# Kernel optimization log

Hardware: AMD Instinct MI355X
Metric: run time of the kernel (lower is better)

Reference implementation:

```python
import jax, jax.numpy as jnp
import numpy as np

NUM_DIM = 384
NUM_HEADS = 12
WIN = 7
L = WIN * WIN
NW = 4
B_ = 1024

def _relative_coords():
    ch, cw = np.meshgrid(np.arange(WIN), np.arange(WIN), indexing='ij')
    coords = np.stack([ch, cw]).reshape(2, -1)  # (2, L)
    rel = coords[:, :, None] - coords[:, None, :]  # (2, L, L)
    rel[0] += WIN - 1
    rel[1] += WIN - 1
    rel[0] *= 2 * WIN - 1
    return jnp.asarray(rel.sum(0), dtype=jnp.int32)  # (L, L)

def setup_inputs() -> dict:
    key = jax.random.key(0)
    k_x, k_m, k_qkv, k_pw, k_pb, k_rb = jax.random.split(key, 6)
    x = jax.random.normal(k_x, (B_, L, NUM_DIM), dtype=jnp.float32)
    mask = jax.random.bernoulli(k_m, 0.5, (NW, L, L))
    qkv_w = jax.random.normal(k_qkv, (3 * NUM_DIM, NUM_DIM), dtype=jnp.float32) * (NUM_DIM ** -0.5)
    proj_w = jax.random.normal(k_pw, (NUM_DIM, NUM_DIM), dtype=jnp.float32) * (NUM_DIM ** -0.5)
    proj_b = jax.random.normal(k_pb, (NUM_DIM,), dtype=jnp.float32) * 0.02
    rel_bias = jax.random.normal(k_rb, ((2 * WIN - 1) * (2 * WIN - 1), NUM_HEADS), dtype=jnp.float32) * 0.2
    rel_coords = _relative_coords()
    return {"x": x, "mask": mask, "qkv_w": qkv_w, "proj_w": proj_w,
            "proj_b": proj_b, "rel_bias": rel_bias, "rel_coords": rel_coords}

def reference(x, mask, qkv_w, proj_w, proj_b, rel_bias, rel_coords):
    Bt, Lx, C = x.shape
    H = NUM_HEADS
    hd = C // H
    scale = float(C) ** 0.5  # faithful: original multiplies by num_dim**0.5
    qkv = (x @ qkv_w.T).reshape(Bt, Lx, 3, H, hd).transpose(2, 0, 3, 1, 4)
    q, k, v = qkv[0], qkv[1], qkv[2]  # each (B_, H, L, hd)
    attn = jnp.einsum('bhqd,bhkd->bhqk', q, k) * scale
    bias = rel_bias[rel_coords].transpose(2, 0, 1)  # (H, L, L)
    attn = attn + bias[None]
    nw = mask.shape[0]
    attn = attn.reshape(-1, nw, H, Lx, Lx)
    attn = jnp.where(mask[None, :, None], jnp.float32(-100.0), attn)
    attn = attn.reshape(Bt, H, Lx, Lx)
    attn = jax.nn.softmax(attn, axis=-1)
    out = jnp.einsum('bhqk,bhkd->bhqd', attn, v)  # (B_, H, L, hd)
    out = out.transpose(0, 2, 1, 3).reshape(Bt, Lx, C)
    return out @ proj_w.T + proj_b
```

## Files before the change

### kernel.cpp

```cpp
#include <hip/hip_runtime.h>
#include <math.h>

#define NUM_B 1024
#define LW 49
#define CD 384
#define NH 12
#define HD 32
#define SCALE_F 19.595917942265423f

typedef unsigned short u16;
typedef unsigned int u32;
typedef __attribute__((ext_vector_type(8))) short short8;
typedef __attribute__((ext_vector_type(8))) _Float16 half8;
typedef __attribute__((ext_vector_type(4))) float floatx4;

static __device__ __forceinline__ u16 f2bf(float f) {
    unsigned u = __float_as_uint(f);
    u += 0x7fffu + ((u >> 16) & 1u);
    return (u16)(u >> 16);
}
static __device__ __forceinline__ float bf2f(u16 s) {
    return __uint_as_float(((unsigned)s) << 16);
}
static __device__ __forceinline__ u16 f2h_bits(float f) {
    _Float16 h = (_Float16)f;
    u16 u;
    __builtin_memcpy(&u, &h, 2);
    return u;
}
static __device__ __forceinline__ void gl_lds16(const u16* g, u16* l) {
    __builtin_amdgcn_global_load_lds(
        (const __attribute__((address_space(1))) void*)g,
        (__attribute__((address_space(3))) void*)l, 16, 0, 0);
}

#define X4 4816896
#define W4 110592
#define P4 36864
#define BM4 49152
__global__ __launch_bounds__(256) void prep(const float* __restrict__ x,
                                            const float* __restrict__ qkv_w,
                                            const float* __restrict__ proj_w,
                                            const float* __restrict__ rel_bias,
                                            const int* __restrict__ rel_coords,
                                            const int* __restrict__ mask,
                                            u16* __restrict__ xbh, u16* __restrict__ xbl,
                                            u16* __restrict__ wbh, u16* __restrict__ wbl,
                                            u16* __restrict__ pfh, u16* __restrict__ pfl,
                                            float* __restrict__ bm) {
    int idx = blockIdx.x * 256 + threadIdx.x;
    if (idx < X4) {
        float4 v = ((const float4*)x)[idx];
        ushort4 h, l;
        h.x = f2bf(v.x); l.x = f2bf(v.x - bf2f(h.x));
        h.y = f2bf(v.y); l.y = f2bf(v.y - bf2f(h.y));
        h.z = f2bf(v.z); l.z = f2bf(v.z - bf2f(h.z));
        h.w = f2bf(v.w); l.w = f2bf(v.w - bf2f(h.w));
        ((ushort4*)xbh)[idx] = h;
        ((ushort4*)xbl)[idx] = l;
    } else if (idx < X4 + W4) {
        int i = idx - X4;
        float4 v = ((const float4*)qkv_w)[i];
        ushort4 h, l;
        h.x = f2bf(v.x); l.x = f2bf(v.x - bf2f(h.x));
        h.y = f2bf(v.y); l.y = f2bf(v.y - bf2f(h.y));
        h.z = f2bf(v.z); l.z = f2bf(v.z - bf2f(h.z));
        h.w = f2bf(v.w); l.w = f2bf(v.w - bf2f(h.w));
        ((ushort4*)wbh)[i] = h;
        ((ushort4*)wbl)[i] = l;
    } else if (idx < X4 + W4 + P4) {
        int i = idx - (X4 + W4);
        float4 v = ((const float4*)proj_w)[i];
        ushort4 h, l;
        h.x = f2h_bits(v.x); l.x = f2h_bits(v.x - (float)(_Float16)v.x);
        h.y = f2h_bits(v.y); l.y = f2h_bits(v.y - (float)(_Float16)v.y);
        h.z = f2h_bits(v.z); l.z = f2h_bits(v.z - (float)(_Float16)v.z);
        h.w = f2h_bits(v.w); l.w = f2h_bits(v.w - (float)(_Float16)v.w);
        ((ushort4*)pfh)[i] = h;
        ((ushort4*)pfl)[i] = l;
    } else if (idx < X4 + W4 + P4 + BM4) {
        int t = idx - (X4 + W4 + P4);
        float4 o;
        float* op = (float*)&o;
#pragma unroll
        for (int i = 0; i < 4; ++i) {
            int j = t * 4 + i;
            int e = j & 63;
            int col = (e & 3) * 16 + (e >> 2);
            int row = (j >> 6) & 63;
            int wh_ = j >> 12;
            int w = wh_ / NH;
            int h = wh_ - w * NH;
            float val = -1.0e30f;
            if (row < LW && col < LW) {
                int ij = row * LW + col;
                val = mask[w * (LW * LW) + ij] ? -1.0e4f
                                               : rel_bias[rel_coords[ij] * NH + h];
            }
            op[i] = val;
        }
        ((float4*)bm)[t] = o;
    }
}

__global__ __launch_bounds__(256) void qkv_gemm(const u16* __restrict__ Ah,
                                                const u16* __restrict__ Al,
                                                const u16* __restrict__ Wh,
                                                const u16* __restrict__ Wl,
                                                u32* __restrict__ qp,
                                                u32* __restrict__ kp,
                                                u16* __restrict__ vp) {
    __shared__ u16 As_h[2][128 * 32];
    __shared__ u16 As_l[2][128 * 32];
    __shared__ u16 Bs_h[2][128 * 32];
    __shared__ u16 Bs_l[2][128 * 32];
    const int tid = threadIdx.x;
    const int w = tid >> 6;
    const int lane = tid & 63;
    const int bid = blockIdx.x;
    const int logical = (bid & 7) * 441 + (bid >> 3);
    const int mt = logical / 9;
    const int nt = logical - mt * 9;
    const int m0 = mt * 128;
    const int n0 = nt * 128;
    const bool vblk = (nt >= 6);
    const int quad = lane >> 4;
    const int lc = lane & 15;
    const int wrow = (w >> 1) << 6;
    const int wcol = (w & 1) << 6;
    const int srow = lane >> 2;
    const int sch = (lane & 3) * 8;

    floatx4 acc[4][4];
#pragma unroll
    for (int a = 0; a < 4; ++a)
#pragma unroll
        for (int b = 0; b < 4; ++b) acc[a][b] = (floatx4){0.f, 0.f, 0.f, 0.f};

    auto stage = [&](int buf, int k0) {
#pragma unroll
        for (int i = 0; i < 2; ++i) {
            const int rb = w * 32 + i * 16;
            const size_t ga = (size_t)(m0 + rb + srow) * CD + k0 + sch;
            const size_t gb = (size_t)(n0 + rb + srow) * CD + k0 + sch;
            const int lof = rb * 32;
            gl_lds16(Ah + ga, As_h[buf] + lof);
            gl_lds16(Wh + gb, Bs_h[buf] + lof);
            if (!vblk) {
                gl_lds16(Al + ga, As_l[buf] + lof);
                gl_lds16(Wl + gb, Bs_l[buf] + lof);
            }
        }
    };

    auto compute = [&](int buf) {
        if (!vblk) {
            short8 af_h[4], af_l[4], bf_h[4], bf_l[4];
#pragma unroll
            for (int t = 0; t < 4; ++t) {
                const int ar = (wrow + t * 16 + lc) * 32 + quad * 8;
                af_h[t] = *(const short8*)(As_h[buf] + ar);
                af_l[t] = *(const short8*)(As_l[buf] + ar);
                const int br = (wcol + t * 16 + lc) * 32 + quad * 8;
                bf_h[t] = *(const short8*)(Bs_h[buf] + br);
                bf_l[t] = *(const short8*)(Bs_l[buf] + br);
            }
#pragma unroll
            for (int tm = 0; tm < 4; ++tm)
#pragma unroll
                for (int tn = 0; tn < 4; ++tn) {
                    acc[tm][tn] = __builtin_amdgcn_mfma_f32_16x16x32_bf16(af_h[tm], bf_h[tn], acc[tm][tn], 0, 0, 0);
                    acc[tm][tn] = __builtin_amdgcn_mfma_f32_16x16x32_bf16(af_h[tm], bf_l[tn], acc[tm][tn], 0, 0, 0);
                    acc[tm][tn] = __builtin_amdgcn_mfma_f32_16x16x32_bf16(af_l[tm], bf_h[tn], acc[tm][tn], 0, 0, 0);
                }
        } else {
            short8 af_h[4], bf_h[4];
#pragma unroll
            for (int t = 0; t < 4; ++t) {
                af_h[t] = *(const short8*)(As_h[buf] + (wrow + t * 16 + lc) * 32 + quad * 8);
                bf_h[t] = *(const short8*)(Bs_h[buf] + (wcol + t * 16 + lc) * 32 + quad * 8);
            }
#pragma unroll
            for (int tm = 0; tm < 4; ++tm)
#pragma unroll
                for (int tn = 0; tn < 4; ++tn)
                    acc[tm][tn] = __builtin_amdgcn_mfma_f32_16x16x32_bf16(af_h[tm], bf_h[tn], acc[tm][tn], 0, 0, 0);
        }
    };

    stage(0, 0);
    __syncthreads();
    for (int t = 0; t < 12; t += 2) {
        stage(1, (t + 1) * 32);
        compute(0);
        __syncthreads();
        if (t + 2 < 12) stage(0, (t + 2) * 32);
        compute(1);
        __syncthreads();
    }

#pragma unroll
    for (int tn = 0; tn < 4; ++tn) {
        const int nst = n0 + wcol + tn * 16;
        const int t = nst / CD;
        const int rem = nst - t * CD;
        const int h = rem >> 5;
        const int db = (rem & 31) + lc;
#pragma unroll
        for (int tm = 0; tm < 4; ++tm)
#pragma unroll
            for (int r = 0; r < 4; ++r) {
                const int m = m0 + wrow + tm * 16 + quad * 4 + r;
                const int b = m / LW;
                const int l = m - b * LW;
                const size_t o = ((((size_t)b * NH + h) * LW + l) << 5) + db;
                const float vv = acc[tm][tn][r];
                if (t == 2) {
                    vp[o] = f2h_bits(vv);
                } else {
                    const unsigned bits = __float_as_uint(vv);
                    const unsigned hi_high = bits & 0xffff0000u;
                    const u16 lo = f2bf(vv - __uint_as_float(hi_high));
                    const u32 packed = hi_high | (u32)lo;
                    if (t == 0) qp[o] = packed; else kp[o] = packed;
                }
            }
    }
}

__global__ __launch_bounds__(256) void proj_gemm(const u16* __restrict__ Af,
                                                 const u16* __restrict__ Wfh,
                                                 const u16* __restrict__ Wfl,
                                                 const float* __restrict__ pb,
                                                 float* __restrict__ outF) {
    __shared__ u16 As_f[2][128 * 32];
    __shared__ u16 Bs_h[2][128 * 32];
    __shared__ u16 Bs_l[2][128 * 32];
    const int tid = threadIdx.x;
    const int w = tid >> 6;
    const int lane = tid & 63;
    const int bid = blockIdx.x;
    const int logical = (bid & 7) * 147 + (bid >> 3);
    const int mt = logical / 3;
    const int nt = logical - mt * 3;
    const int m0 = mt * 128;
    const int n0 = nt * 128;
    const int quad = lane >> 4;
    const int lc = lane & 15;
    const int wrow = (w >> 1) << 6;
    const int wcol = (w & 1) << 6;
    const int srow = lane >> 2;
    const int sch = (lane & 3) * 8;

    floatx4 acc[4][4];
#pragma unroll
    for (int a = 0; a < 4; ++a)
#pragma unroll
        for (int b = 0; b < 4; ++b) acc[a][b] = (floatx4){0.f, 0.f, 0.f, 0.f};

    auto stage = [&](int buf, int k0) {
#pragma unroll
        for (int i = 0; i < 2; ++i) {
            const int rb = w * 32 + i * 16;
            const size_t ga = (size_t)(m0 + rb + srow) * CD + k0 + sch;
            const size_t gb = (size_t)(n0 + rb + srow) * CD + k0 + sch;
            const int lof = rb * 32;
            gl_lds16(Af + ga, As_f[buf] + lof);
            gl_lds16(Wfh + gb, Bs_h[buf] + lof);
            gl_lds16(Wfl + gb, Bs_l[buf] + lof);
        }
    };

    auto compute = [&](int buf) {
        half8 af[4], bh[4], bl[4];
#pragma unroll
        for (int t = 0; t < 4; ++t) {
            af[t] = *(const half8*)(As_f[buf] + (wrow + t * 16 + lc) * 32 + quad * 8);
            const int br = (wcol + t * 16 + lc) * 32 + quad * 8;
            bh[t] = *(const half8*)(Bs_h[buf] + br);
            bl[t] = *(const half8*)(Bs_l[buf] + br);
        }
#pragma unroll
        for (int tm = 0; tm < 4; ++tm)
#pragma unroll
            for (int tn = 0; tn < 4; ++tn) {
                acc[tm][tn] = __builtin_amdgcn_mfma_f32_16x16x32_f16(af[tm], bh[tn], acc[tm][tn], 0, 0, 0);
                acc[tm][tn] = __builtin_amdgcn_mfma_f32_16x16x32_f16(af[tm], bl[tn], acc[tm][tn], 0, 0, 0);
            }
    };

    stage(0, 0);
    __syncthreads();
    for (int t = 0; t < 12; t += 2) {
        stage(1, (t + 1) * 32);
        compute(0);
        __syncthreads();
        if (t + 2 < 12) stage(0, (t + 2) * 32);
        compute(1);
        __syncthreads();
    }

#pragma unroll
    for (int tn = 0; tn < 4; ++tn) {
        const int n = n0 + wcol + tn * 16 + lc;
        const float bias = pb[n];
#pragma unroll
        for (int tm = 0; tm < 4; ++tm)
#pragma unroll
            for (int r = 0; r < 4; ++r) {
                const int m = m0 + wrow + tm * 16 + quad * 4 + r;
                outF[(size_t)m * CD + n] = acc[tm][tn][r] + bias;
            }
    }
}

__global__ __launch_bounds__(64) void attn_mfma(const u32* __restrict__ qp,
                                                const u32* __restrict__ kp,
                                                const u16* __restrict__ vh,
                                                const float* __restrict__ bm,
                                                u16* __restrict__ aof) {
    const int bh = blockIdx.x;
    const int b = bh / NH;
    const int h = bh - b * NH;
    const int lane = threadIdx.x;
    const int quad = lane >> 4;
    const int lc = lane & 15;
    __shared__ u16 Vt[32 * 72];
    __shared__ u16 Ps[64 * 72];

    const size_t base = (size_t)bh * (LW * HD);

    short8 aQh[4], aQl[4], bKh[4], bKl[4];
#pragma unroll
    for (int t = 0; t < 4; ++t) {
        int row = t * 16 + lc; if (row > 48) row = 48;
        const size_t o = base + (size_t)row * HD + quad * 8;
        uint4 q0 = *(const uint4*)(qp + o);
        uint4 q1 = *(const uint4*)(qp + o + 4);
        uint4 k0 = *(const uint4*)(kp + o);
        uint4 k1 = *(const uint4*)(kp + o + 4);
        unsigned qv[8] = {q0.x, q0.y, q0.z, q0.w, q1.x, q1.y, q1.z, q1.w};
        unsigned kv[8] = {k0.x, k0.y, k0.z, k0.w, k1.x, k1.y, k1.z, k1.w};
#pragma unroll
        for (int e = 0; e < 8; ++e) {
            aQh[t][e] = (short)(qv[e] >> 16);
            aQl[t][e] = (short)(qv[e] & 0xffffu);
            bKh[t][e] = (short)(kv[e] >> 16);
            bKl[t][e] = (short)(kv[e] & 0xffffu);
        }
    }
#pragma unroll
    for (int it = 0; it < 4; ++it) {
        const int idx = lane + it * 64;
        const int j = idx >> 2;
        const int jc = j > 48 ? 48 : j;
        const int ch = (idx & 3) * 8;
        short8 vv = *(const short8*)(vh + base + (size_t)jc * HD + ch);
#pragma unroll
        for (int e = 0; e < 8; ++e) Vt[(ch + e) * 72 + j] = (u16)vv[e];
    }

    floatx4 acc[4][4];
#pragma unroll
    for (int a = 0; a < 4; ++a)
#pragma unroll
        for (int c = 0; c < 4; ++c) acc[a][c] = (floatx4){0.f, 0.f, 0.f, 0.f};
#pragma unroll
    for (int tm = 0; tm < 4; ++tm)
#pragma unroll
        for (int tn = 0; tn < 4; ++tn) {
            acc[tm][tn] = __builtin_amdgcn_mfma_f32_16x16x32_bf16(aQh[tm], bKh[tn], acc[tm][tn], 0, 0, 0);
            acc[tm][tn] = __builtin_amdgcn_mfma_f32_16x16x32_bf16(aQh[tm], bKl[tn], acc[tm][tn], 0, 0, 0);
            acc[tm][tn] = __builtin_amdgcn_mfma_f32_16x16x32_bf16(aQl[tm], bKh[tn], acc[tm][tn], 0, 0, 0);
        }

    const float* bmp = bm + (((size_t)(b & 3) * NH + h) << 12);
#pragma unroll
    for (int tm = 0; tm < 4; ++tm)
#pragma unroll
        for (int r = 0; r < 4; ++r) {
            const int row = tm * 16 + quad * 4 + r;
            const float4 bv = *(const float4*)(bmp + row * 64 + lc * 4);
            const float s0 = fmaf(acc[tm][0][r], SCALE_F, bv.x);
            const float s1 = fmaf(acc[tm][1][r], SCALE_F, bv.y);
            const float s2 = fmaf(acc[tm][2][r], SCALE_F, bv.z);
            const float s3 = fmaf(acc[tm][3][r], SCALE_F, bv.w);
            float mx = fmaxf(fmaxf(s0, s1), fmaxf(s2, s3));
#pragma unroll
            for (int off = 1; off < 16; off <<= 1) mx = fmaxf(mx, __shfl_xor(mx, off));
            const float e0 = __expf(s0 - mx);
            const float e1 = __expf(s1 - mx);
            const float e2 = __expf(s2 - mx);
            const float e3 = __expf(s3 - mx);
            float sum = (e0 + e1) + (e2 + e3);
#pragma unroll
            for (int off = 1; off < 16; off <<= 1) sum += __shfl_xor(sum, off);
            const float inv = __builtin_amdgcn_rcpf(sum);
            Ps[row * 72 +  0 + lc] = f2h_bits(e0 * inv);
            Ps[row * 72 + 16 + lc] = f2h_bits(e1 * inv);
            Ps[row * 72 + 32 + lc] = f2h_bits(e2 * inv);
            Ps[row * 72 + 48 + lc] = f2h_bits(e3 * inv);
        }

    __syncthreads();

    floatx4 o[4][2];
#pragma unroll
    for (int a = 0; a < 4; ++a) { o[a][0] = (floatx4){0.f,0.f,0.f,0.f}; o[a][1] = (floatx4){0.f,0.f,0.f,0.f}; }
#pragma unroll
    for (int ks = 0; ks < 2; ++ks) {
        const half8 bV0 = *(const half8*)(Vt + (lc) * 72 + ks * 32 + quad * 8);
        const half8 bV1 = *(const half8*)(Vt + (16 + lc) * 72 + ks * 32 + quad * 8);
#pragma unroll
        for (int tm = 0; tm < 4; ++tm) {
            const half8 aP = *(const half8*)(Ps + (tm * 16 + lc) * 72 + ks * 32 + quad * 8);
            o[tm][0] = __builtin_amdgcn_mfma_f32_16x16x32_f16(aP, bV0, o[tm][0], 0, 0, 0);
            o[tm][1] = __builtin_amdgcn_mfma_f32_16x16x32_f16(aP, bV1, o[tm][1], 0, 0, 0);
        }
    }
#pragma unroll
    for (int tm = 0; tm < 4; ++tm)
#pragma unroll
        for (int r = 0; r < 4; ++r) {
            const int i = tm * 16 + quad * 4 + r;
            if (i < LW) {
#pragma unroll
                for (int tn = 0; tn < 2; ++tn) {
                    const size_t mm = ((size_t)b * LW + i) * CD + h * HD + tn * 16 + lc;
                    aof[mm] = f2h_bits(o[tm][tn][r]);
                }
            }
        }
}

extern "C" void kernel_launch(void* const* d_in, const int* in_sizes, int n_in,
                              void* d_out, int out_size, void* d_ws, size_t ws_size,
                              hipStream_t stream) {
    const float* x          = (const float*)d_in[0];
    const int*   mask       = (const int*)d_in[1];
    const float* qkv_w      = (const float*)d_in[2];
    const float* proj_w     = (const float*)d_in[3];
    const float* proj_b     = (const float*)d_in[4];
    const float* rel_bias   = (const float*)d_in[5];
    const int*   rel_coords = (const int*)d_in[6];
    float* out = (float*)d_out;

    const size_t S = (size_t)NUM_B * NH * LW * HD;
    u16* xbh = (u16*)d_ws;
    u16* xbl = xbh + S;
    u32* kp  = (u32*)(xbl + S);
    u16* vh  = (u16*)(kp + S);
    u16* wbh = vh + S;
    u16* wbl = wbh + 442368;
    u16* pfh = wbl + 442368;
    u16* pfl = pfh + 147456;
    float* bm = (float*)(pfl + 147456);
    u32* qp = (u32*)d_out;
    u16* aof = xbh;

    prep<<<dim3(19584), dim3(256), 0, stream>>>(x, qkv_w, proj_w, rel_bias, rel_coords,
                                                mask, xbh, xbl, wbh, wbl, pfh, pfl, bm);
    qkv_gemm<<<dim3(3528), dim3(256), 0, stream>>>(xbh, xbl, wbh, wbl, qp, kp, vh);
    attn_mfma<<<dim3(NUM_B * NH), dim3(64), 0, stream>>>(qp, kp, vh, bm, aof);
    proj_gemm<<<dim3(1176), dim3(256), 0, stream>>>(aof, pfh, pfl, proj_b, out);
}
```

Measured before the change: 404.5 us.

## Deepen GEMM double-buffer pipeline with explicit vmcnt waits and raw barriers

Both GEMM kernels now issue loads for the first two k-tiles up front and prefetch the next tile into a buffer right after it has been consumed. __syncthreads is replaced with hand-placed s_waitcnt vmcnt/lgkmcnt and s_barrier, so only the older stage's global-to-LDS loads must land before compute. The aim is to keep two tiles of loads in flight and overlap them with the MFMA work. The vmcnt constants are hard-coded to the number of loads each stage issues (different for the vblk path), so a mismatch would silently read incomplete LDS data.

```diff
diff --git a/kernel.cpp b/kernel.cpp
--- a/kernel.cpp
+++ b/kernel.cpp
@@ -13,6 +13,10 @@
 typedef __attribute__((ext_vector_type(8))) short short8;
 typedef __attribute__((ext_vector_type(8))) _Float16 half8;
 typedef __attribute__((ext_vector_type(4))) float floatx4;
+
+#define ASM_VMCNT(n) asm volatile("s_waitcnt vmcnt(" #n ")" ::: "memory")
+#define ASM_LGKM0()  asm volatile("s_waitcnt lgkmcnt(0)" ::: "memory")
+#define BAR()        __builtin_amdgcn_s_barrier()
 
 static __device__ __forceinline__ u16 f2bf(float f) {
     unsigned u = __float_as_uint(f);
@@ -189,14 +193,33 @@
     };
 
     stage(0, 0);
-    __syncthreads();
-    for (int t = 0; t < 12; t += 2) {
-        stage(1, (t + 1) * 32);
-        compute(0);
-        __syncthreads();
-        if (t + 2 < 12) stage(0, (t + 2) * 32);
-        compute(1);
-        __syncthreads();
+    stage(1, 32);
+    if (!vblk) {
+#pragma unroll
+        for (int t = 0; t < 12; t += 2) {
+            ASM_VMCNT(8); BAR();
+            compute(0);
+            ASM_LGKM0(); BAR();
+            if (t + 2 < 12) { stage(0, (t + 2) * 32); ASM_VMCNT(8); }
+            else            { ASM_VMCNT(0); }
+            BAR();
+            compute(1);
+            ASM_LGKM0(); BAR();
+            if (t + 2 < 12) stage(1, (t + 3) * 32);
+        }
+    } else {
+#pragma unroll
+        for (int t = 0; t < 12; t += 2) {
+            ASM_VMCNT(4); BAR();
+            compute(0);
+            ASM_LGKM0(); BAR();
+            if (t + 2 < 12) { stage(0, (t + 2) * 32); ASM_VMCNT(4); }
+            else            { ASM_VMCNT(0); }
+            BAR();
+            compute(1);
+            ASM_LGKM0(); BAR();
+            if (t + 2 < 12) stage(1, (t + 3) * 32);
+        }
     }
 
 #pragma unroll
@@ -290,14 +313,18 @@
     };
 
     stage(0, 0);
-    __syncthreads();
+    stage(1, 32);
+#pragma unroll
     for (int t = 0; t < 12; t += 2) {
-        stage(1, (t + 1) * 32);
+        ASM_VMCNT(6); BAR();
         compute(0);
-        __syncthreads();
-        if (t + 2 < 12) stage(0, (t + 2) * 32);
+        ASM_LGKM0(); BAR();
+        if (t + 2 < 12) { stage(0, (t + 2) * 32); ASM_VMCNT(6); }
+        else            { ASM_VMCNT(0); }
+        BAR();
         compute(1);
-        __syncthreads();
+        ASM_LGKM0(); BAR();
+        if (t + 2 < 12) stage(1, (t + 3) * 32);
     }
 
 #pragma unroll
```

After: 388.0 us. 4.1% less time.

## Triple-buffer GEMM LDS staging and load low-part operands directly from global

Applied to the files above, without the earlier changes.

Both the QKV and projection GEMMs move from double buffering with two __syncthreads per pair of steps to a three-stage ring. Each k-step now uses an explicit vmcnt wait and one barrier, and keeps two stages of loads in flight. The low-precision correction operands (Al/Wl, Wfl) no longer go through LDS and are read straight from global memory into registers. Launch bounds request three blocks per CU. This cuts LDS footprint and barrier stalls, at the cost of uncoalesced per-lane global reads for the low parts and hand-counted vmcnt that must match the number of outstanding loads.

```diff
diff --git a/kernel.cpp b/kernel.cpp
--- a/kernel.cpp
+++ b/kernel.cpp
@@ -13,6 +13,9 @@
 typedef __attribute__((ext_vector_type(8))) short short8;
 typedef __attribute__((ext_vector_type(8))) _Float16 half8;
 typedef __attribute__((ext_vector_type(4))) float floatx4;
+
+#define ASM_VMCNT(n) asm volatile("s_waitcnt vmcnt(" #n ")" ::: "memory")
+#define BAR()        __builtin_amdgcn_s_barrier()
 
 static __device__ __forceinline__ u16 f2bf(float f) {
     unsigned u = __float_as_uint(f);
@@ -103,17 +106,15 @@
     }
 }
 
-__global__ __launch_bounds__(256) void qkv_gemm(const u16* __restrict__ Ah,
-                                                const u16* __restrict__ Al,
-                                                const u16* __restrict__ Wh,
-                                                const u16* __restrict__ Wl,
-                                                u32* __restrict__ qp,
-                                                u32* __restrict__ kp,
-                                                u16* __restrict__ vp) {
-    __shared__ u16 As_h[2][128 * 32];
-    __shared__ u16 As_l[2][128 * 32];
-    __shared__ u16 Bs_h[2][128 * 32];
-    __shared__ u16 Bs_l[2][128 * 32];
+__global__ __launch_bounds__(256, 3) void qkv_gemm(const u16* __restrict__ Ah,
+                                                   const u16* __restrict__ Al,
+                                                   const u16* __restrict__ Wh,
+                                                   const u16* __restrict__ Wl,
+                                                   u32* __restrict__ qp,
+                                                   u32* __restrict__ kp,
+                                                   u16* __restrict__ vp) {
+    __shared__ u16 As_h[3][128 * 32];
+    __shared__ u16 Bs_h[3][128 * 32];
     const int tid = threadIdx.x;
     const int w = tid >> 6;
     const int lane = tid & 63;
@@ -141,44 +142,53 @@
 #pragma unroll
         for (int i = 0; i < 2; ++i) {
             const int rb = w * 32 + i * 16;
-            const size_t ga = (size_t)(m0 + rb + srow) * CD + k0 + sch;
-            const size_t gb = (size_t)(n0 + rb + srow) * CD + k0 + sch;
-            const int lof = rb * 32;
-            gl_lds16(Ah + ga, As_h[buf] + lof);
-            gl_lds16(Wh + gb, Bs_h[buf] + lof);
-            if (!vblk) {
-                gl_lds16(Al + ga, As_l[buf] + lof);
-                gl_lds16(Wl + gb, Bs_l[buf] + lof);
-            }
+            gl_lds16(Ah + (size_t)(m0 + rb + srow) * CD + k0 + sch, As_h[buf] + rb * 32);
+            gl_lds16(Wh + (size_t)(n0 + rb + srow) * CD + k0 + sch, Bs_h[buf] + rb * 32);
         }
     };
 
-    auto compute = [&](int buf) {
+    stage(0, 0);
+    stage(1, 32);
+
+#pragma unroll
+    for (int t = 0; t < 12; ++t) {
+        if (t == 11) { ASM_VMCNT(0); } else { ASM_VMCNT(4); }
+        BAR();
+        const int buf = t % 3;
+        const int k0 = t * 32;
         if (!vblk) {
-            short8 af_h[4], af_l[4], bf_h[4], bf_l[4];
-#pragma unroll
-            for (int t = 0; t < 4; ++t) {
-                const int ar = (wrow + t * 16 + lc) * 32 + quad * 8;
-                af_h[t] = *(const short8*)(As_h[buf] + ar);
-                af_l[t] = *(const short8*)(As_l[buf] + ar);
-                const int br = (wcol + t * 16 + lc) * 32 + quad * 8;
-                bf_h[t] = *(const short8*)(Bs_h[buf] + br);
-                bf_l[t] = *(const short8*)(Bs_l[buf] + br);
+            short8 af_l[4], bf_l[4];
+#pragma unroll
+            for (int tt = 0; tt < 4; ++tt) {
+                af_l[tt] = *(const short8*)(Al + (size_t)(m0 + wrow + tt * 16 + lc) * CD + k0 + quad * 8);
+                bf_l[tt] = *(const short8*)(Wl + (size_t)(n0 + wcol + tt * 16 + lc) * CD + k0 + quad * 8);
+            }
+            if (t + 2 < 12) stage((t + 2) % 3, (t + 2) * 32);
+            short8 af_h[4], bf_h[4];
+#pragma unroll
+            for (int tt = 0; tt < 4; ++tt) {
+                af_h[tt] = *(const short8*)(As_h[buf] + (wrow + tt * 16 + lc) * 32 + quad * 8);
+                bf_h[tt] = *(const short8*)(Bs_h[buf] + (wcol + tt * 16 + lc) * 32 + quad * 8);
             }
 #pragma unroll
             for (int tm = 0; tm < 4; ++tm)
 #pragma unroll
+                for (int tn = 0; tn < 4; ++tn)
+                    acc[tm][tn] = __builtin_amdgcn_mfma_f32_16x16x32_bf16(af_h[tm], bf_h[tn], acc[tm][tn], 0, 0, 0);
+#pragma unroll
+            for (int tm = 0; tm < 4; ++tm)
+#pragma unroll
                 for (int tn = 0; tn < 4; ++tn) {
-                    acc[tm][tn] = __builtin_amdgcn_mfma_f32_16x16x32_bf16(af_h[tm], bf_h[tn], acc[tm][tn], 0, 0, 0);
                     acc[tm][tn] = __builtin_amdgcn_mfma_f32_16x16x32_bf16(af_h[tm], bf_l[tn], acc[tm][tn], 0, 0, 0);
                     acc[tm][tn] = __builtin_amdgcn_mfma_f32_16x16x32_bf16(af_l[tm], bf_h[tn], acc[tm][tn], 0, 0, 0);
                 }
         } else {
+            if (t + 2 < 12) stage((t + 2) % 3, (t + 2) * 32);
             short8 af_h[4], bf_h[4];
 #pragma unroll
-            for (int t = 0; t < 4; ++t) {
-                af_h[t] = *(const short8*)(As_h[buf] + (wrow + t * 16 + lc) * 32 + quad * 8);
-                bf_h[t] = *(const short8*)(Bs_h[buf] + (wcol + t * 16 + lc) * 32 + quad * 8);
+            for (int tt = 0; tt < 4; ++tt) {
+                af_h[tt] = *(const short8*)(As_h[buf] + (wrow + tt * 16 + lc) * 32 + quad * 8);
+                bf_h[tt] = *(const short8*)(Bs_h[buf] + (wcol + tt * 16 + lc) * 32 + quad * 8);
             }
 #pragma unroll
             for (int tm = 0; tm < 4; ++tm)
@@ -186,17 +196,6 @@
                 for (int tn = 0; tn < 4; ++tn)
                     acc[tm][tn] = __builtin_amdgcn_mfma_f32_16x16x32_bf16(af_h[tm], bf_h[tn], acc[tm][tn], 0, 0, 0);
         }
-    };
-
-    stage(0, 0);
-    __syncthreads();
-    for (int t = 0; t < 12; t += 2) {
-        stage(1, (t + 1) * 32);
-        compute(0);
-        __syncthreads();
-        if (t + 2 < 12) stage(0, (t + 2) * 32);
-        compute(1);
-        __syncthreads();
     }
 
 #pragma unroll
@@ -228,14 +227,13 @@
     }
 }
 
-__global__ __launch_bounds__(256) void proj_gemm(const u16* __restrict__ Af,
-                                                 const u16* __restrict__ Wfh,
-                                                 const u16* __restrict__ Wfl,
-                                                 const float* __restrict__ pb,
-                                                 float* __restrict__ outF) {
-    __shared__ u16 As_f[2][128 * 32];
-    __shared__ u16 Bs_h[2][128 * 32];
-    __shared__ u16 Bs_l[2][128 * 32];
+__global__ __launch_bounds__(256, 3) void proj_gemm(const u16* __restrict__ Af,
+                                                    const u16* __restrict__ Wfh,
+                                                    const u16* __restrict__ Wfl,
+                                                    const float* __restrict__ pb,
+                                                    float* __restrict__ outF) {
+    __shared__ u16 As_f[3][128 * 32];
+    __shared__ u16 Bs_h[3][128 * 32];
     const int tid = threadIdx.x;
     const int w = tid >> 6;
     const int lane = tid & 63;
@@ -262,42 +260,41 @@
 #pragma unroll
         for (int i = 0; i < 2; ++i) {
             const int rb = w * 32 + i * 16;
-            const size_t ga = (size_t)(m0 + rb + srow) * CD + k0 + sch;
-            const size_t gb = (size_t)(n0 + rb + srow) * CD + k0 + sch;
-            const int lof = rb * 32;
-            gl_lds16(Af + ga, As_f[buf] + lof);
-            gl_lds16(Wfh + gb, Bs_h[buf] + lof);
-            gl_lds16(Wfl + gb, Bs_l[buf] + lof);
+            gl_lds16(Af + (size_t)(m0 + rb + srow) * CD + k0 + sch, As_f[buf] + rb * 32);
+            gl_lds16(Wfh + (size_t)(n0 + rb + srow) * CD + k0 + sch, Bs_h[buf] + rb * 32);
         }
     };
 
-    auto compute = [&](int buf) {
-        half8 af[4], bh[4], bl[4];
-#pragma unroll
-        for (int t = 0; t < 4; ++t) {
-            af[t] = *(const half8*)(As_f[buf] + (wrow + t * 16 + lc) * 32 + quad * 8);
-            const int br = (wcol + t * 16 + lc) * 32 + quad * 8;
-            bh[t] = *(const half8*)(Bs_h[buf] + br);
-            bl[t] = *(const half8*)(Bs_l[buf] + br);
+    stage(0, 0);
+    stage(1, 32);
+
+#pragma unroll
+    for (int t = 0; t < 12; ++t) {
+        if (t == 11) { ASM_VMCNT(0); } else { ASM_VMCNT(4); }
+        BAR();
+        const int buf = t % 3;
+        const int k0 = t * 32;
+        half8 bl[4];
+#pragma unroll
+        for (int tt = 0; tt < 4; ++tt)
+            bl[tt] = *(const half8*)(Wfl + (size_t)(n0 + wcol + tt * 16 + lc) * CD + k0 + quad * 8);
+        if (t + 2 < 12) stage((t + 2) % 3, (t + 2) * 32);
+        half8 af[4], bh[4];
+#pragma unroll
+        for (int tt = 0; tt < 4; ++tt) {
+            af[tt] = *(const half8*)(As_f[buf] + (wrow + tt * 16 + lc) * 32 + quad * 8);
+            bh[tt] = *(const half8*)(Bs_h[buf] + (wcol + tt * 16 + lc) * 32 + quad * 8);
         }
 #pragma unroll
         for (int tm = 0; tm < 4; ++tm)
 #pragma unroll
-            for (int tn = 0; tn < 4; ++tn) {
+            for (int tn = 0; tn < 4; ++tn)
                 acc[tm][tn] = __builtin_amdgcn_mfma_f32_16x16x32_f16(af[tm], bh[tn], acc[tm][tn], 0, 0, 0);
+#pragma unroll
+        for (int tm = 0; tm < 4; ++tm)
+#pragma unroll
+            for (int tn = 0; tn < 4; ++tn)
                 acc[tm][tn] = __builtin_amdgcn_mfma_f32_16x16x32_f16(af[tm], bl[tn], acc[tm][tn], 0, 0, 0);
-            }
-    };
-
-    stage(0, 0);
-    __syncthreads();
-    for (int t = 0; t < 12; t += 2) {
-        stage(1, (t + 1) * 32);
-        compute(0);
-        __syncthreads();
-        if (t + 2 < 12) stage(0, (t + 2) * 32);
-        compute(1);
-        __syncthreads();
     }
 
 #pragma unroll
```

After: 642.8 us. 1.59x slower.
